# Kernel optimization log

Hardware: AMD Instinct MI355X
Metric: run time of the kernel (lower is better)

Reference implementation:

```python
import jax, jax.numpy as jnp
import numpy as np


def setup_inputs() -> dict:
    key = jax.random.key(0)
    k1, k2, k3, k4, k5 = jax.random.split(key, 5)
    B_, S, D_in, D_out, R = 2, 2048, 4096, 4096, 4
    return {
        "x": jax.random.normal(k1, (B_, S, D_in), dtype=jnp.float32),
        "weight": jax.random.normal(k2, (D_out, D_in), dtype=jnp.float32) * 0.02,
        "bias": jax.random.normal(k3, (D_out,), dtype=jnp.float32) * 0.02,
        "scale_A": jax.random.normal(k4, (D_out, R), dtype=jnp.float32),
        "scale_B": jax.random.normal(k5, (R, D_in), dtype=jnp.float32),
        "rank_magnitude": jnp.ones((R,), dtype=jnp.float32),
    }


def reference(x, weight, bias, scale_A, scale_B, rank_magnitude):
    # Factored forward with default bound_mode='tanh', A_max=B_max=1.0, pad=0:
    #   y = sum_k g_k * A[:, k] * ((x * B[k]) @ Q.T) + bias
    Q = weight  # snapped_mode=None, _Q=None -> Q = raw weight
    A = jnp.tanh(scale_A)            # [O, R]
    Bm = jnp.tanh(scale_B)           # [R, I] (pad == 0)
    Ag = A * rank_magnitude[None, :]  # fold g_k into A -> [O, R]
    # [b,s,i] x [r,i] -> [b,s,r,i]; contract i with Q [o,i]; weight by Ag [o,r]
    y = jnp.einsum("bsi,ri,oi,or->bso", x, Bm, Q, Ag)
    return y + bias
```

## Files before the change

### kernel.cpp

```cpp
#include <hip/hip_runtime.h>
#include <hip/hip_bf16.h>

typedef __attribute__((ext_vector_type(8))) short bf16x8;
typedef __attribute__((ext_vector_type(4))) float f32x4;
typedef __attribute__((ext_vector_type(4))) short s16x4;

#define M_DIM 4096
#define N_DIM 4096
#define K_DIM 4096
#define R_DIM 4

__device__ __forceinline__ short to_bf16(float f) {
    __hip_bfloat16 h = __float2bfloat16(f);
    return *reinterpret_cast<short*>(&h);
}

__global__ __launch_bounds__(256)
void k_prep(const float* __restrict__ sA, const float* __restrict__ sB,
            const float* __restrict__ g, float* __restrict__ tB,
            float* __restrict__ tAg) {
    int i = blockIdx.x * 256 + threadIdx.x;
    if (i < R_DIM * K_DIM) {
        tB[i] = tanhf(sB[i]);
    } else {
        int j = i - R_DIM * K_DIM;
        tAg[j] = tanhf(sA[j]) * g[j & 3];
    }
}

__global__ __launch_bounds__(256)
void k_xcast(const float* __restrict__ x, __hip_bfloat16* __restrict__ xb) {
    const size_t i = ((size_t)blockIdx.x * 256 + threadIdx.x) << 3;
    float4 u = *(const float4*)&x[i];
    float4 v = *(const float4*)&x[i + 4];
    bf16x8 pk;
    pk[0] = to_bf16(u.x); pk[1] = to_bf16(u.y);
    pk[2] = to_bf16(u.z); pk[3] = to_bf16(u.w);
    pk[4] = to_bf16(v.x); pk[5] = to_bf16(v.y);
    pk[6] = to_bf16(v.z); pk[7] = to_bf16(v.w);
    *(bf16x8*)&xb[i] = pk;
}

__global__ __launch_bounds__(256)
void k_weff(const float* __restrict__ w, const float* __restrict__ tB,
            const float* __restrict__ tAg, __hip_bfloat16* __restrict__ weff) {
    const int o = blockIdx.x;
    const float a0 = tAg[o * 4 + 0];
    const float a1 = tAg[o * 4 + 1];
    const float a2 = tAg[o * 4 + 2];
    const float a3 = tAg[o * 4 + 3];
#pragma unroll
    for (int it = 0; it < 4; ++it) {
        const int i = (it * 256 + (int)threadIdx.x) << 2;
        float4 wv = *(const float4*)&w[(size_t)o * K_DIM + i];
        float4 b0 = *(const float4*)&tB[0 * K_DIM + i];
        float4 b1 = *(const float4*)&tB[1 * K_DIM + i];
        float4 b2 = *(const float4*)&tB[2 * K_DIM + i];
        float4 b3 = *(const float4*)&tB[3 * K_DIM + i];
        float s0 = a0 * b0.x + a1 * b1.x + a2 * b2.x + a3 * b3.x;
        float s1 = a0 * b0.y + a1 * b1.y + a2 * b2.y + a3 * b3.y;
        float s2 = a0 * b0.z + a1 * b1.z + a2 * b2.z + a3 * b3.z;
        float s3 = a0 * b0.w + a1 * b1.w + a2 * b2.w + a3 * b3.w;
        s16x4 pk;
        pk[0] = to_bf16(wv.x * s0);
        pk[1] = to_bf16(wv.y * s1);
        pk[2] = to_bf16(wv.z * s2);
        pk[3] = to_bf16(wv.w * s3);
        *(s16x4*)&weff[(size_t)o * K_DIM + i] = pk;
    }
}

#define MFMA(A, B, C) __builtin_amdgcn_mfma_f32_16x16x32_bf16(A, B, C, 0, 0, 0)

#define RA0 0
#define RA1 32768
#define RA2 65536
#define SA0 0
#define SA1 16384
#define SA2 32768
#define SB0 49152
#define SB1 65536

#define RD_A8(ab, qq) \
    aA = *(const bf16x8*)(LA0 + (ab) + (qq)*4096 + 0); \
    aB = *(const bf16x8*)(LA1 + (ab) + (qq)*4096 + 0); \
    aC = *(const bf16x8*)(LA0 + (ab) + (qq)*4096 + 2048); \
    aD = *(const bf16x8*)(LA1 + (ab) + (qq)*4096 + 2048); \
    aE = *(const bf16x8*)(LA0 + (ab) + (qq)*4096 + 4096); \
    aF = *(const bf16x8*)(LA1 + (ab) + (qq)*4096 + 4096); \
    aG = *(const bf16x8*)(LA0 + (ab) + (qq)*4096 + 6144); \
    aH = *(const bf16x8*)(LA1 + (ab) + (qq)*4096 + 6144);

#define RD_B8(bb) \
    b0 = *(const bf16x8*)(LB0 + (bb) + 0);    b1 = *(const bf16x8*)(LB1 + (bb) + 0); \
    b2 = *(const bf16x8*)(LB0 + (bb) + 2048); b3 = *(const bf16x8*)(LB1 + (bb) + 2048); \
    b4 = *(const bf16x8*)(LB0 + (bb) + 4096); b5 = *(const bf16x8*)(LB1 + (bb) + 4096); \
    b6 = *(const bf16x8*)(LB0 + (bb) + 6144); b7 = *(const bf16x8*)(LB1 + (bb) + 6144);

#define MFMA32(qq) \
     \
    acc[2*(qq)+0][0] = MFMA(aA, b0, acc[2*(qq)+0][0]); \
    acc[2*(qq)+0][1] = MFMA(aA, b2, acc[2*(qq)+0][1]); \
    acc[2*(qq)+0][2] = MFMA(aA, b4, acc[2*(qq)+0][2]); \
    acc[2*(qq)+0][3] = MFMA(aA, b6, acc[2*(qq)+0][3]); \
    acc[2*(qq)+1][0] = MFMA(aC, b0, acc[2*(qq)+1][0]); \
    acc[2*(qq)+1][1] = MFMA(aC, b2, acc[2*(qq)+1][1]); \
    acc[2*(qq)+1][2] = MFMA(aC, b4, acc[2*(qq)+1][2]); \
    acc[2*(qq)+1][3] = MFMA(aC, b6, acc[2*(qq)+1][3]); \
    acc[2*(qq)+2][0] = MFMA(aE, b0, acc[2*(qq)+2][0]); \
    acc[2*(qq)+2][1] = MFMA(aE, b2, acc[2*(qq)+2][1]); \
    acc[2*(qq)+2][2] = MFMA(aE, b4, acc[2*(qq)+2][2]); \
    acc[2*(qq)+2][3] = MFMA(aE, b6, acc[2*(qq)+2][3]); \
    acc[2*(qq)+3][0] = MFMA(aG, b0, acc[2*(qq)+3][0]); \
    acc[2*(qq)+3][1] = MFMA(aG, b2, acc[2*(qq)+3][1]); \
    acc[2*(qq)+3][2] = MFMA(aG, b4, acc[2*(qq)+3][2]); \
    acc[2*(qq)+3][3] = MFMA(aG, b6, acc[2*(qq)+3][3]); \
     \
    acc[2*(qq)+0][0] = MFMA(aB, b1, acc[2*(qq)+0][0]); \
    acc[2*(qq)+0][1] = MFMA(aB, b3, acc[2*(qq)+0][1]); \
    acc[2*(qq)+0][2] = MFMA(aB, b5, acc[2*(qq)+0][2]); \
    acc[2*(qq)+0][3] = MFMA(aB, b7, acc[2*(qq)+0][3]); \
    acc[2*(qq)+1][0] = MFMA(aD, b1, acc[2*(qq)+1][0]); \
    acc[2*(qq)+1][1] = MFMA(aD, b3, acc[2*(qq)+1][1]); \
    acc[2*(qq)+1][2] = MFMA(aD, b5, acc[2*(qq)+1][2]); \
    acc[2*(qq)+1][3] = MFMA(aD, b7, acc[2*(qq)+1][3]); \
    acc[2*(qq)+2][0] = MFMA(aF, b1, acc[2*(qq)+2][0]); \
    acc[2*(qq)+2][1] = MFMA(aF, b3, acc[2*(qq)+2][1]); \
    acc[2*(qq)+2][2] = MFMA(aF, b5, acc[2*(qq)+2][2]); \
    acc[2*(qq)+2][3] = MFMA(aF, b7, acc[2*(qq)+2][3]); \
    acc[2*(qq)+3][0] = MFMA(aH, b1, acc[2*(qq)+3][0]); \
    acc[2*(qq)+3][1] = MFMA(aH, b3, acc[2*(qq)+3][1]); \
    acc[2*(qq)+3][2] = MFMA(aH, b5, acc[2*(qq)+3][2]); \
    acc[2*(qq)+3][3] = MFMA(aH, b7, acc[2*(qq)+3][3]);

#define VM4 asm volatile("s_waitcnt vmcnt(4)" ::: "memory")

#define PH4(READS_STMT, STAGE_STMT, VM_STMT, qq) \
    { READS_STMT; \
      STAGE_STMT; \
      VM_STMT; \
      __builtin_amdgcn_s_barrier(); \
      asm volatile("s_waitcnt lgkmcnt(0)" ::: "memory"); \
      __builtin_amdgcn_sched_barrier(0); \
      __builtin_amdgcn_s_setprio(1); \
      MFMA32(qq); \
      __builtin_amdgcn_s_setprio(0); }

#define ITER4(RAu, RAv, SAu, SAw, KT1, KT2, KT3) \
    PH4(RD_A8(RAu, 0); RD_B8(0),     STGT(gB, KT1, SB1), , 0) \
    PH4(RD_A8(RAu, 2),               STGT(gA, KT2, SAw), VM4, 2) \
    PH4(RD_A8(RAv, 0); RD_B8(32768), STGT(gB, KT2, SB0), , 0) \
    PH4(RD_A8(RAv, 2),               STGT(gA, KT3, SAu), VM4, 2)

__global__ __launch_bounds__(512, 2)
void k_gemm8(const __hip_bfloat16* __restrict__ xb,
             const __hip_bfloat16* __restrict__ weff,
             const float* __restrict__ bias, float* __restrict__ out) {
    __shared__ short lds[81920];

    const int tid  = threadIdx.x;
    const int lane = tid & 63;
    const int wid  = tid >> 6;
    const int wr   = wid >> 2;
    const int wc   = wid & 3;
    const int l15  = lane & 15;
    const int cb0  = (lane >> 4) << 4;

    const int bid = blockIdx.x;
    const int swz = (bid & 7) * 32 + (bid >> 3);
    const int m0g = (swz >> 4) << 8;
    const int n0g = (swz & 15) << 8;

    const int mask = (l15 & 7) << 4;
    const int cbs0 = cb0 ^ mask;
    const int cbs1 = (cb0 + 64) ^ mask;
    const char* LAb = (const char*)lds + wr * 16384 + l15 * 128;
    const char* LA0 = LAb + cbs0;
    const char* LA1 = LAb + cbs1;
    const char* LBb = (const char*)lds + 98304 + (wc >> 1) * 16384 +
                      ((wc & 1) * 64 + l15) * 128;
    const char* LB0 = LBb + cbs0;
    const char* LB1 = LBb + cbs1;

    const int rowL  = tid >> 3;
    const int colbL = ((tid * 16) & 127) ^ ((rowL & 7) << 4);
    const __hip_bfloat16* gA = xb   + ((size_t)(m0g + rowL) << 12) + (colbL >> 1);
    const __hip_bfloat16* gB = weff + ((size_t)(n0g + rowL) << 12) + (colbL >> 1);

    auto STGT = [&](const __hip_bfloat16* gbase, int k0, int dstShort) {
#pragma unroll
        for (int p = 0; p < 4; ++p) {
            __builtin_amdgcn_global_load_lds(
                (const __attribute__((address_space(1))) void*)(gbase + p * 262144 + k0),
                (__attribute__((address_space(3))) void*)&lds[dstShort + p * 4096 + tid * 8],
                16, 0, 0);
        }
    };

    f32x4 acc[8][4] = {};
    bf16x8 aA, aB, aC, aD, aE, aF, aG, aH;
    bf16x8 b0, b1, b2, b3, b4, b5, b6, b7;

    STGT(gB, 0, SB0);
    STGT(gA, 0, SA0);
    STGT(gA, 64, SA1);
    asm volatile("s_waitcnt vmcnt(0)" ::: "memory");
    __builtin_amdgcn_s_barrier();
    __builtin_amdgcn_sched_barrier(0);

    for (int j = 0; j < 10; ++j) {
        const int t = 6 * j;
        ITER4(RA0, RA1, SA0, SA2, (t + 1) * 64, (t + 2) * 64, (t + 3) * 64);
        ITER4(RA2, RA0, SA2, SA1, (t + 3) * 64, (t + 4) * 64, (t + 5) * 64);
        ITER4(RA1, RA2, SA1, SA0, (t + 5) * 64, (t + 6) * 64, (t + 7) * 64);
    }
    ITER4(RA0, RA1, SA0, SA2, 61 * 64, 62 * 64, 63 * 64);
    ITER4(RA2, RA0, SA2, SA1, 63 * 64, 63 * 64, 63 * 64);

#pragma unroll
    for (int n = 0; n < 4; ++n) {
        const int col = n0g + wc * 64 + n * 16 + l15;
        const float bv = bias[col];
#pragma unroll
        for (int m = 0; m < 8; ++m) {
            const int rbase = m0g + wr * 128 + m * 16 + ((lane >> 4) << 2);
#pragma unroll
            for (int j2 = 0; j2 < 4; ++j2)
                out[(size_t)(rbase + j2) * N_DIM + col] = acc[m][n][j2] + bv;
        }
    }
}

extern "C" void kernel_launch(void* const* d_in, const int* in_sizes, int n_in,
                              void* d_out, int out_size, void* d_ws, size_t ws_size,
                              hipStream_t stream) {
    const float* x    = (const float*)d_in[0];
    const float* w    = (const float*)d_in[1];
    const float* bias = (const float*)d_in[2];
    const float* sA   = (const float*)d_in[3];
    const float* sB   = (const float*)d_in[4];
    const float* g    = (const float*)d_in[5];
    float* out = (float*)d_out;

    __hip_bfloat16* weff = (__hip_bfloat16*)d_ws;
    __hip_bfloat16* xb   = (__hip_bfloat16*)((char*)d_ws + (32ull << 20));
    float* tB  = (float*)((char*)d_ws + (64ull << 20));
    float* tAg = (float*)((char*)d_ws + (64ull << 20) + (R_DIM * K_DIM * 4));

    k_prep<<<dim3((2 * R_DIM * K_DIM) / 256), dim3(256), 0, stream>>>(sA, sB, g, tB, tAg);
    k_xcast<<<dim3((M_DIM * K_DIM) / (256 * 8)), dim3(256), 0, stream>>>(x, xb);
    k_weff<<<dim3(N_DIM), dim3(256), 0, stream>>>(w, tB, tAg, weff);
    k_gemm8<<<dim3((M_DIM / 256) * (N_DIM / 256)), dim3(512), 0, stream>>>(xb, weff, bias, out);
}
```

Measured before the change: 152.2 us.

## Merge x-cast and weight-prep kernels and split LDS reads by k-half

The x bf16 cast and the effective-weight construction now run as one launch, with blocks dispatched by index, removing one kernel launch and its tail. In the GEMM main loop, LDS fragment reads are split into two k-halves with a partial lgkmcnt wait, so the first 16 MFMAs can start while the second half's reads are still in flight. This adds scheduling barriers and relies on the lgkmcnt counts matching the number of outstanding reads.

Result: faster. 148.6 us (-2.4%).

```diff
diff --git a/kernel.cpp b/kernel.cpp
--- a/kernel.cpp
+++ b/kernel.cpp
@@ -29,44 +29,45 @@
 }
 
 __global__ __launch_bounds__(256)
-void k_xcast(const float* __restrict__ x, __hip_bfloat16* __restrict__ xb) {
-    const size_t i = ((size_t)blockIdx.x * 256 + threadIdx.x) << 3;
-    float4 u = *(const float4*)&x[i];
-    float4 v = *(const float4*)&x[i + 4];
-    bf16x8 pk;
-    pk[0] = to_bf16(u.x); pk[1] = to_bf16(u.y);
-    pk[2] = to_bf16(u.z); pk[3] = to_bf16(u.w);
-    pk[4] = to_bf16(v.x); pk[5] = to_bf16(v.y);
-    pk[6] = to_bf16(v.z); pk[7] = to_bf16(v.w);
-    *(bf16x8*)&xb[i] = pk;
-}
-
-__global__ __launch_bounds__(256)
-void k_weff(const float* __restrict__ w, const float* __restrict__ tB,
+void k_pre2(const float* __restrict__ x, __hip_bfloat16* __restrict__ xb,
+            const float* __restrict__ w, const float* __restrict__ tB,
             const float* __restrict__ tAg, __hip_bfloat16* __restrict__ weff) {
-    const int o = blockIdx.x;
-    const float a0 = tAg[o * 4 + 0];
-    const float a1 = tAg[o * 4 + 1];
-    const float a2 = tAg[o * 4 + 2];
-    const float a3 = tAg[o * 4 + 3];
-#pragma unroll
-    for (int it = 0; it < 4; ++it) {
-        const int i = (it * 256 + (int)threadIdx.x) << 2;
-        float4 wv = *(const float4*)&w[(size_t)o * K_DIM + i];
-        float4 b0 = *(const float4*)&tB[0 * K_DIM + i];
-        float4 b1 = *(const float4*)&tB[1 * K_DIM + i];
-        float4 b2 = *(const float4*)&tB[2 * K_DIM + i];
-        float4 b3 = *(const float4*)&tB[3 * K_DIM + i];
-        float s0 = a0 * b0.x + a1 * b1.x + a2 * b2.x + a3 * b3.x;
-        float s1 = a0 * b0.y + a1 * b1.y + a2 * b2.y + a3 * b3.y;
-        float s2 = a0 * b0.z + a1 * b1.z + a2 * b2.z + a3 * b3.z;
-        float s3 = a0 * b0.w + a1 * b1.w + a2 * b2.w + a3 * b3.w;
-        s16x4 pk;
-        pk[0] = to_bf16(wv.x * s0);
-        pk[1] = to_bf16(wv.y * s1);
-        pk[2] = to_bf16(wv.z * s2);
-        pk[3] = to_bf16(wv.w * s3);
-        *(s16x4*)&weff[(size_t)o * K_DIM + i] = pk;
+    const int bid = blockIdx.x;
+    if (bid < 8192) {
+        const size_t i = ((size_t)bid * 256 + threadIdx.x) << 3;
+        float4 u = *(const float4*)&x[i];
+        float4 v = *(const float4*)&x[i + 4];
+        bf16x8 pk;
+        pk[0] = to_bf16(u.x); pk[1] = to_bf16(u.y);
+        pk[2] = to_bf16(u.z); pk[3] = to_bf16(u.w);
+        pk[4] = to_bf16(v.x); pk[5] = to_bf16(v.y);
+        pk[6] = to_bf16(v.z); pk[7] = to_bf16(v.w);
+        *(bf16x8*)&xb[i] = pk;
+    } else {
+        const int o = bid - 8192;
+        const float a0 = tAg[o * 4 + 0];
+        const float a1 = tAg[o * 4 + 1];
+        const float a2 = tAg[o * 4 + 2];
+        const float a3 = tAg[o * 4 + 3];
+#pragma unroll
+        for (int it = 0; it < 4; ++it) {
+            const int i = (it * 256 + (int)threadIdx.x) << 2;
+            float4 wv = *(const float4*)&w[(size_t)o * K_DIM + i];
+            float4 b0 = *(const float4*)&tB[0 * K_DIM + i];
+            float4 b1 = *(const float4*)&tB[1 * K_DIM + i];
+            float4 b2 = *(const float4*)&tB[2 * K_DIM + i];
+            float4 b3 = *(const float4*)&tB[3 * K_DIM + i];
+            float s0 = a0 * b0.x + a1 * b1.x + a2 * b2.x + a3 * b3.x;
+            float s1 = a0 * b0.y + a1 * b1.y + a2 * b2.y + a3 * b3.y;
+            float s2 = a0 * b0.z + a1 * b1.z + a2 * b2.z + a3 * b3.z;
+            float s3 = a0 * b0.w + a1 * b1.w + a2 * b2.w + a3 * b3.w;
+            s16x4 pk;
+            pk[0] = to_bf16(wv.x * s0);
+            pk[1] = to_bf16(wv.y * s1);
+            pk[2] = to_bf16(wv.z * s2);
+            pk[3] = to_bf16(wv.w * s3);
+            *(s16x4*)&weff[(size_t)o * K_DIM + i] = pk;
+        }
     }
 }
 
@@ -81,24 +82,31 @@
 #define SB0 49152
 #define SB1 65536
 
-#define RD_A8(ab, qq) \
+#define RD_A_KS0(ab, qq) \
     aA = *(const bf16x8*)(LA0 + (ab) + (qq)*4096 + 0); \
+    aC = *(const bf16x8*)(LA0 + (ab) + (qq)*4096 + 2048); \
+    aE = *(const bf16x8*)(LA0 + (ab) + (qq)*4096 + 4096); \
+    aG = *(const bf16x8*)(LA0 + (ab) + (qq)*4096 + 6144);
+
+#define RD_A_KS1(ab, qq) \
     aB = *(const bf16x8*)(LA1 + (ab) + (qq)*4096 + 0); \
-    aC = *(const bf16x8*)(LA0 + (ab) + (qq)*4096 + 2048); \
     aD = *(const bf16x8*)(LA1 + (ab) + (qq)*4096 + 2048); \
-    aE = *(const bf16x8*)(LA0 + (ab) + (qq)*4096 + 4096); \
     aF = *(const bf16x8*)(LA1 + (ab) + (qq)*4096 + 4096); \
-    aG = *(const bf16x8*)(LA0 + (ab) + (qq)*4096 + 6144); \
     aH = *(const bf16x8*)(LA1 + (ab) + (qq)*4096 + 6144);
 
-#define RD_B8(bb) \
-    b0 = *(const bf16x8*)(LB0 + (bb) + 0);    b1 = *(const bf16x8*)(LB1 + (bb) + 0); \
-    b2 = *(const bf16x8*)(LB0 + (bb) + 2048); b3 = *(const bf16x8*)(LB1 + (bb) + 2048); \
-    b4 = *(const bf16x8*)(LB0 + (bb) + 4096); b5 = *(const bf16x8*)(LB1 + (bb) + 4096); \
-    b6 = *(const bf16x8*)(LB0 + (bb) + 6144); b7 = *(const bf16x8*)(LB1 + (bb) + 6144);
-
-#define MFMA32(qq) \
-     \
+#define RD_B_KS0(bb) \
+    b0 = *(const bf16x8*)(LB0 + (bb) + 0); \
+    b2 = *(const bf16x8*)(LB0 + (bb) + 2048); \
+    b4 = *(const bf16x8*)(LB0 + (bb) + 4096); \
+    b6 = *(const bf16x8*)(LB0 + (bb) + 6144);
+
+#define RD_B_KS1(bb) \
+    b1 = *(const bf16x8*)(LB1 + (bb) + 0); \
+    b3 = *(const bf16x8*)(LB1 + (bb) + 2048); \
+    b5 = *(const bf16x8*)(LB1 + (bb) + 4096); \
+    b7 = *(const bf16x8*)(LB1 + (bb) + 6144);
+
+#define MFMA16_KS0(qq) \
     acc[2*(qq)+0][0] = MFMA(aA, b0, acc[2*(qq)+0][0]); \
     acc[2*(qq)+0][1] = MFMA(aA, b2, acc[2*(qq)+0][1]); \
     acc[2*(qq)+0][2] = MFMA(aA, b4, acc[2*(qq)+0][2]); \
@@ -114,8 +122,9 @@
     acc[2*(qq)+3][0] = MFMA(aG, b0, acc[2*(qq)+3][0]); \
     acc[2*(qq)+3][1] = MFMA(aG, b2, acc[2*(qq)+3][1]); \
     acc[2*(qq)+3][2] = MFMA(aG, b4, acc[2*(qq)+3][2]); \
-    acc[2*(qq)+3][3] = MFMA(aG, b6, acc[2*(qq)+3][3]); \
-     \
+    acc[2*(qq)+3][3] = MFMA(aG, b6, acc[2*(qq)+3][3]);
+
+#define MFMA16_KS1(qq) \
     acc[2*(qq)+0][0] = MFMA(aB, b1, acc[2*(qq)+0][0]); \
     acc[2*(qq)+0][1] = MFMA(aB, b3, acc[2*(qq)+0][1]); \
     acc[2*(qq)+0][2] = MFMA(aB, b5, acc[2*(qq)+0][2]); \
@@ -134,23 +143,35 @@
     acc[2*(qq)+3][3] = MFMA(aH, b7, acc[2*(qq)+3][3]);
 
 #define VM4 asm volatile("s_waitcnt vmcnt(4)" ::: "memory")
-
-#define PH4(READS_STMT, STAGE_STMT, VM_STMT, qq) \
-    { READS_STMT; \
+#define SB0F __builtin_amdgcn_sched_barrier(0)
+
+#define PH4(RD_KS0, RD_KS1, STAGE_STMT, VM_STMT, qq, LGK_ASM) \
+    { RD_KS0; \
+      SB0F; \
+      RD_KS1; \
       STAGE_STMT; \
       VM_STMT; \
       __builtin_amdgcn_s_barrier(); \
+      asm volatile(LGK_ASM ::: "memory"); \
+      SB0F; \
+      __builtin_amdgcn_s_setprio(1); \
+      MFMA16_KS0(qq); \
+      __builtin_amdgcn_s_setprio(0); \
       asm volatile("s_waitcnt lgkmcnt(0)" ::: "memory"); \
-      __builtin_amdgcn_sched_barrier(0); \
+      SB0F; \
       __builtin_amdgcn_s_setprio(1); \
-      MFMA32(qq); \
+      MFMA16_KS1(qq); \
       __builtin_amdgcn_s_setprio(0); }
 
 #define ITER4(RAu, RAv, SAu, SAw, KT1, KT2, KT3) \
-    PH4(RD_A8(RAu, 0); RD_B8(0),     STGT(gB, KT1, SB1), , 0) \
-    PH4(RD_A8(RAu, 2),               STGT(gA, KT2, SAw), VM4, 2) \
-    PH4(RD_A8(RAv, 0); RD_B8(32768), STGT(gB, KT2, SB0), , 0) \
-    PH4(RD_A8(RAv, 2),               STGT(gA, KT3, SAu), VM4, 2)
+    PH4(RD_A_KS0(RAu, 0); RD_B_KS0(0), RD_A_KS1(RAu, 0); RD_B_KS1(0), \
+        STGT(gB, KT1, SB1), , 0, "s_waitcnt lgkmcnt(8)") \
+    PH4(RD_A_KS0(RAu, 2), RD_A_KS1(RAu, 2), \
+        STGT(gA, KT2, SAw), VM4, 2, "s_waitcnt lgkmcnt(4)") \
+    PH4(RD_A_KS0(RAv, 0); RD_B_KS0(32768), RD_A_KS1(RAv, 0); RD_B_KS1(32768), \
+        STGT(gB, KT2, SB0), , 0, "s_waitcnt lgkmcnt(8)") \
+    PH4(RD_A_KS0(RAv, 2), RD_A_KS1(RAv, 2), \
+        STGT(gA, KT3, SAu), VM4, 2, "s_waitcnt lgkmcnt(4)")
 
 __global__ __launch_bounds__(512, 2)
 void k_gemm8(const __hip_bfloat16* __restrict__ xb,
@@ -206,7 +227,7 @@
     STGT(gA, 64, SA1);
     asm volatile("s_waitcnt vmcnt(0)" ::: "memory");
     __builtin_amdgcn_s_barrier();
-    __builtin_amdgcn_sched_barrier(0);
+    SB0F;
 
     for (int j = 0; j < 10; ++j) {
         const int t = 6 * j;
@@ -248,7 +269,6 @@
     float* tAg = (float*)((char*)d_ws + (64ull << 20) + (R_DIM * K_DIM * 4));
 
     k_prep<<<dim3((2 * R_DIM * K_DIM) / 256), dim3(256), 0, stream>>>(sA, sB, g, tB, tAg);
-    k_xcast<<<dim3((M_DIM * K_DIM) / (256 * 8)), dim3(256), 0, stream>>>(x, xb);
-    k_weff<<<dim3(N_DIM), dim3(256), 0, stream>>>(w, tB, tAg, weff);
+    k_pre2<<<dim3(8192 + N_DIM), dim3(256), 0, stream>>>(x, xb, w, tB, tAg, weff);
     k_gemm8<<<dim3((M_DIM / 256) * (N_DIM / 256)), dim3(512), 0, stream>>>(xb, weff, bias, out);
 }
```
